# Optimization experiments

Hardware: AMD Instinct MI355X
Metric: run time of the kernel (lower is better)

Reference implementation:

```python
import jax, jax.numpy as jnp
import numpy as np

B, H, W, C = 4, 224, 224, 256
HEADS = 8
WIN = 7
N = WIN * WIN  # 49 tokens per window
MLP_HID = 4 * C
EPS = 1e-5


def _rel_index(w):
    coords = np.stack(np.meshgrid(np.arange(w), np.arange(w), indexing='ij'))  # (2,w,w)
    cf = coords.reshape(2, -1)                       # (2, w*w)
    rc = cf[:, :, None] - cf[:, None, :]             # (2, N, N)
    rc = rc.transpose(1, 2, 0).astype(np.int64)      # (N, N, 2)
    rc[:, :, 0] += w - 1
    rc[:, :, 1] += w - 1
    rc[:, :, 0] *= 2 * w - 1
    return jnp.asarray(rc.sum(-1), dtype=jnp.int32)  # (N, N)


def setup_inputs() -> dict:
    key = jax.random.key(0)
    ks = jax.random.split(key, 6)
    std = 0.02
    return {
        'x': jax.random.normal(ks[0], (B, H, W, C), dtype=jnp.float32),
        'norm1_g': jnp.ones((C,), jnp.float32),
        'norm1_b': jnp.zeros((C,), jnp.float32),
        'qkv_w': jax.random.normal(ks[1], (3 * C, C), jnp.float32) * std,
        'qkv_b': jnp.zeros((3 * C,), jnp.float32),
        'bias_table': jax.random.normal(ks[2], ((2 * WIN - 1) ** 2, HEADS), jnp.float32) * std,
        'proj_w': jax.random.normal(ks[3], (C, C), jnp.float32) * std,
        'proj_b': jnp.zeros((C,), jnp.float32),
        'norm2_g': jnp.ones((C,), jnp.float32),
        'norm2_b': jnp.zeros((C,), jnp.float32),
        'fc1_w': jax.random.normal(ks[4], (MLP_HID, C), jnp.float32) * std,
        'fc1_b': jnp.zeros((MLP_HID,), jnp.float32),
        'fc2_w': jax.random.normal(ks[5], (C, MLP_HID), jnp.float32) * std,
        'fc2_b': jnp.zeros((C,), jnp.float32),
        'rel_index': _rel_index(WIN),
    }


def _layernorm(x, g, b):
    mu = jnp.mean(x, axis=-1, keepdims=True)
    var = jnp.mean(jnp.square(x - mu), axis=-1, keepdims=True)
    return (x - mu) * jax.lax.rsqrt(var + EPS) * g + b


def reference(x, norm1_g, norm1_b, qkv_w, qkv_b, bias_table, proj_w, proj_b,
              norm2_g, norm2_b, fc1_w, fc1_b, fc2_w, fc2_b, rel_index):
    Bc, Hc, Wc, Cc = x.shape
    d = Cc // HEADS
    scale = d ** -0.5
    nh, nw = Hc // WIN, Wc // WIN

    shortcut = x
    h = _layernorm(x, norm1_g, norm1_b)

    # window_partition: (B,H,W,C) -> (B*nW, N, C)
    wins = h.reshape(Bc, nh, WIN, nw, WIN, Cc).transpose(0, 1, 3, 2, 4, 5)
    wins = wins.reshape(-1, N, Cc)

    # qkv projection and split into heads
    qkv = wins @ qkv_w.T + qkv_b                                  # (Bw, N, 3C)
    qkv = qkv.reshape(-1, N, 3, HEADS, d).transpose(2, 0, 3, 1, 4)  # (3, Bw, h, N, d)
    q, k, v = qkv[0], qkv[1], qkv[2]

    attn = jnp.einsum('bhnd,bhmd->bhnm', q, k) * scale            # (Bw, h, N, N)
    bias = bias_table[rel_index.reshape(-1)].reshape(N, N, HEADS).transpose(2, 0, 1)
    attn = jax.nn.softmax(attn + bias[None], axis=-1)

    o = jnp.einsum('bhnm,bhmd->bhnd', attn, v)                    # (Bw, h, N, d)
    o = o.transpose(0, 2, 1, 3).reshape(-1, N, Cc)
    o = o @ proj_w.T + proj_b

    # window_reverse: (B*nW, N, C) -> (B,H,W,C)
    o = o.reshape(Bc, nh, nw, WIN, WIN, Cc).transpose(0, 1, 3, 2, 4, 5)
    o = o.reshape(Bc, Hc, Wc, Cc)

    x = shortcut + o
    h2 = _layernorm(x, norm2_g, norm2_b)
    m = jax.nn.gelu(h2 @ fc1_w.T + fc1_b, approximate=False) @ fc2_w.T + fc2_b
    return x + m
```

## Files before the change

### kernel.cpp

```cpp
#include <hip/hip_runtime.h>

typedef unsigned short u16;
typedef __bf16 bf16x8 __attribute__((ext_vector_type(8)));
typedef float f32x4 __attribute__((ext_vector_type(4)));

#define TOKENS 200704
#define QK_ELEMS 51380224UL

__device__ __forceinline__ u16 f2b(float f) {
    __bf16 h = (__bf16)f;
    return __builtin_bit_cast(u16, h);
}

__device__ __forceinline__ int win2tok(int gm) {
    const int win = gm / 49, pos = gm - win * 49;
    const int b = win >> 10, wrem = win & 1023, wy = wrem >> 5, wx = wrem & 31;
    const int y = wy * 7 + pos / 7, x = wx * 7 + pos % 7;
    return b * 50176 + y * 224 + x;
}

#define GLDS(g, l) __builtin_amdgcn_global_load_lds( \
    (const __attribute__((address_space(1))) void*)(g), \
    (__attribute__((address_space(3))) void*)(l), 16, 0, 0)

#define MFMA __builtin_amdgcn_mfma_f32_16x16x32_bf16

template<int EPI, int WR, int WC>
__global__ __launch_bounds__(512, 4)
void gemm_t(const u16* __restrict__ A, const u16* __restrict__ W,
            const float* __restrict__ bias, int nt, int K, long moff,
            u16* __restrict__ outb, float* __restrict__ outf,
            const float* __restrict__ res,
            const float* __restrict__ g2, const float* __restrict__ b2,
            u16* __restrict__ h2o)
{
    constexpr int BM = WR * 64, BN = WC * 64;
    constexpr int ACH = BM / 16;
    constexpr int TCH = (BM + BN) / 16;
    __shared__ u16 As[3][BM * 32];
    __shared__ u16 Bs[3][BN * 32];
    __shared__ float red[EPI == 1 ? 2 * 128 * 4 : 1];

    const int tid  = threadIdx.x;
    const int wave = tid >> 6, lane = tid & 63;

    const int nwg = gridDim.x, bidO = blockIdx.x;
    const int qq = nwg >> 3, rr = nwg & 7;
    const int xcd = bidO & 7, idxx = bidO >> 3;
    const int bid = (xcd < rr) ? (xcd * (qq + 1) + idxx)
                               : (rr * (qq + 1) + (xcd - rr) * qq + idxx);

    const int bm = bid / nt, bn = bid % nt;
    const long m0 = (long)bm * BM;
    const int  n0 = bn * BN;
    const int wr = wave / WC, wc = wave % WC;
    const int lr = lane & 15, lg = lane >> 4;
    const int ccol_s = (((lane & 3) ^ ((lane >> 3) & 3)) * 8);
    const int swzr = (lg ^ ((lr >> 1) & 3)) * 8;

    f32x4 acc[4][4] = {};

    auto stage = [&](int buf, int k0) {
#pragma unroll
        for (int p = 0; p < TCH / 8; ++p) {
            const int q = p * 8 + wave;
            const int rq = (q < ACH) ? q : q - ACH;
            const int row = rq * 16 + (lane >> 2);
            if (q < ACH)
                GLDS(A + (m0 + row) * (long)K + k0 + ccol_s, &As[buf][rq * 512]);
            else
                GLDS(W + (long)(n0 + row) * K + k0 + ccol_s, &Bs[buf][rq * 512]);
        }
    };

    auto compute = [&](int buf) {
        bf16x8 af[4], bfr[4];
#pragma unroll
        for (int fm = 0; fm < 4; ++fm)
            af[fm] = *reinterpret_cast<const bf16x8*>(
                &As[buf][(wr * 64 + fm * 16 + lr) * 32 + swzr]);
#pragma unroll
        for (int fn = 0; fn < 4; ++fn)
            bfr[fn] = *reinterpret_cast<const bf16x8*>(
                &Bs[buf][(wc * 64 + fn * 16 + lr) * 32 + swzr]);
        __builtin_amdgcn_s_setprio(1);
#pragma unroll
        for (int fm = 0; fm < 4; ++fm)
#pragma unroll
            for (int fn = 0; fn < 4; ++fn)
                acc[fm][fn] = MFMA(af[fm], bfr[fn], acc[fm][fn], 0, 0, 0);
        __builtin_amdgcn_s_setprio(0);
    };

    const int nk = K >> 5;
    stage(0, 0);
    stage(1, 32);
    stage(2, 64);
    int k = 96;
    int buf = 0;
    for (int t = 0; t < nk; ++t) {
        if (t + 2 < nk)      asm volatile("s_waitcnt vmcnt(6)" ::: "memory");
        else if (t + 1 < nk) asm volatile("s_waitcnt vmcnt(3)" ::: "memory");
        else                 asm volatile("s_waitcnt vmcnt(0)" ::: "memory");
        __builtin_amdgcn_s_barrier();
        __builtin_amdgcn_sched_barrier(0);
        compute(buf);
        __builtin_amdgcn_s_barrier();
        __builtin_amdgcn_sched_barrier(0);
        if (t + 3 < nk) {
            stage(buf, k); k += 32;
            __builtin_amdgcn_sched_barrier(0);
        }
        buf = (buf == 2) ? 0 : buf + 1;
    }

    if constexpr (EPI == 0 || EPI == 2) {
        u16* st = &As[0][0];
        float bb4[4], sc4[4];
#pragma unroll
        for (int fn = 0; fn < 4; ++fn) {
            const int n = n0 + wc * 64 + fn * 16 + lr;
            bb4[fn] = bias[n];
            sc4[fn] = (EPI == 0 && (n >> 8) == 0) ? 0.17677669529663687f : 1.0f;
        }
        const size_t secbase = (EPI == 0)
            ? (size_t)(n0 >> 8) * QK_ELEMS + (size_t)(n0 & 255) : 0;
#pragma unroll
        for (int h = 0; h < 2; ++h) {
            if ((wr >> 1) == h) {
#pragma unroll
                for (int fm = 0; fm < 4; ++fm) {
#pragma unroll
                    for (int r = 0; r < 4; ++r) {
                        const int lrow = (wr & 1) * 64 + fm * 16 + lg * 4 + r;
                        const int swb = ((lrow >> 2) & 3) << 1;
#pragma unroll
                        for (int fn = 0; fn < 4; ++fn) {
                            const int col = wc * 64 + fn * 16 + lr;
                            const int cs = (col >> 3) ^ swb;
                            float v = acc[fm][fn][r] + bb4[fn];
                            u16 w;
                            if (EPI == 0) {
                                w = f2b(v * sc4[fn]);
                            } else {
                                const float s = v * (1.5957691216f + 0.07135481627f * v * v);
                                w = f2b(v * __builtin_amdgcn_rcpf(1.0f + __expf(-s)));
                            }
                            st[lrow * 128 + cs * 8 + (col & 7)] = w;
                        }
                    }
                }
            }
            asm volatile("s_waitcnt lgkmcnt(0)" ::: "memory");
            __builtin_amdgcn_s_barrier();
#pragma unroll
            for (int it = 0; it < 4; ++it) {
                const int u = it * 512 + tid;
                const int row = u >> 4, chunk = u & 15;
                const int cs = chunk ^ (((row >> 2) & 3) << 1);
                const bf16x8 val = *reinterpret_cast<const bf16x8*>(st + row * 128 + cs * 8);
                const long m = m0 + h * 128 + row;
                if (EPI == 0) {
                    *reinterpret_cast<bf16x8*>(outb + secbase + m * 256 + (chunk << 3)) = val;
                } else {
                    *reinterpret_cast<bf16x8*>(outb + m * 1024 + n0 + (chunk << 3)) = val;
                }
            }
            if (h == 0) {
                asm volatile("s_waitcnt lgkmcnt(0)" ::: "memory");
                __builtin_amdgcn_s_barrier();
            }
        }
    } else if constexpr (EPI == 1) {
        float g2c[4], b2c[4];
#pragma unroll
        for (int fn = 0; fn < 4; ++fn) {
            const int n = wc * 64 + fn * 16 + lr;
            g2c[fn] = g2[n]; b2c[fn] = b2[n];
        }
#pragma unroll
        for (int fm = 0; fm < 4; ++fm) {
#pragma unroll
            for (int r = 0; r < 4; ++r) {
                const long m = m0 + wr * 64 + fm * 16 + lg * 4 + r;
                const size_t trow = (size_t)win2tok((int)m) * 256;
                float s = 0.f, s2 = 0.f;
#pragma unroll
                for (int fn = 0; fn < 4; ++fn) {
                    const int n = wc * 64 + fn * 16 + lr;
                    const float x2 = acc[fm][fn][r] + bias[n] + res[trow + n];
                    acc[fm][fn][r] = x2;
                    outf[trow + n] = x2;
                    s += x2; s2 += x2 * x2;
                }
#pragma unroll
                for (int d = 1; d < 16; d <<= 1) { s += __shfl_xor(s, d); s2 += __shfl_xor(s2, d); }
                if (lr == 0) {
                    const int tok = wr * 64 + fm * 16 + lg * 4 + r;
                    red[(0 * 128 + tok) * 4 + wc] = s;
                    red[(1 * 128 + tok) * 4 + wc] = s2;
                }
            }
        }
        __syncthreads();
#pragma unroll
        for (int fm = 0; fm < 4; ++fm) {
#pragma unroll
            for (int r = 0; r < 4; ++r) {
                const int tok = wr * 64 + fm * 16 + lg * 4 + r;
                const float s = red[(0 * 128 + tok) * 4 + 0] + red[(0 * 128 + tok) * 4 + 1]
                              + red[(0 * 128 + tok) * 4 + 2] + red[(0 * 128 + tok) * 4 + 3];
                const float q = red[(1 * 128 + tok) * 4 + 0] + red[(1 * 128 + tok) * 4 + 1]
                              + red[(1 * 128 + tok) * 4 + 2] + red[(1 * 128 + tok) * 4 + 3];
                const float mu = s * 0.00390625f;
                const float rs = rsqrtf(q * 0.00390625f - mu * mu + 1e-5f);
                const long m = m0 + tok;
#pragma unroll
                for (int fn = 0; fn < 4; ++fn) {
                    const int n = wc * 64 + fn * 16 + lr;
                    h2o[m * 256 + n] = f2b((acc[fm][fn][r] - mu) * rs * g2c[fn] + b2c[fn]);
                }
            }
        }
    } else {
#pragma unroll
        for (int fm = 0; fm < 4; ++fm) {
#pragma unroll
            for (int r = 0; r < 4; ++r) {
                const long m = m0 + wr * 64 + fm * 16 + lg * 4 + r;
                const size_t trow = (size_t)win2tok((int)(m + moff)) * 256;
#pragma unroll
                for (int fn = 0; fn < 4; ++fn) {
                    const int n = n0 + wc * 64 + fn * 16 + lr;
                    outf[trow + n] += acc[fm][fn][r] + bias[n];
                }
            }
        }
    }
}

__global__ __launch_bounds__(256)
void layernorm_k(const float* __restrict__ in, const float* __restrict__ g,
                 const float* __restrict__ bb, u16* __restrict__ out)
{
    const int token = blockIdx.x * 4 + (threadIdx.x >> 6);
    const int lane = threadIdx.x & 63;
    const float4 v = *reinterpret_cast<const float4*>(in + (size_t)token * 256 + lane * 4);
    float s  = v.x + v.y + v.z + v.w;
    float s2 = v.x * v.x + v.y * v.y + v.z * v.z + v.w * v.w;
#pragma unroll
    for (int m = 1; m < 64; m <<= 1) { s += __shfl_xor(s, m); s2 += __shfl_xor(s2, m); }
    const float mu  = s * (1.0f / 256.0f);
    const float var = s2 * (1.0f / 256.0f) - mu * mu;
    const float rs  = rsqrtf(var + 1e-5f);
    const float4 gv = *reinterpret_cast<const float4*>(g + lane * 4);
    const float4 bv = *reinterpret_cast<const float4*>(bb + lane * 4);
    ushort4 o;
    o.x = f2b((v.x - mu) * rs * gv.x + bv.x);
    o.y = f2b((v.y - mu) * rs * gv.y + bv.y);
    o.z = f2b((v.z - mu) * rs * gv.z + bv.z);
    o.w = f2b((v.w - mu) * rs * gv.w + bv.w);
    const int b = token / 50176, rem = token % 50176;
    const int y = rem / 224, x = rem % 224;
    const int win = (b * 32 + y / 7) * 32 + x / 7;
    const int pos = (y % 7) * 7 + (x % 7);
    const size_t wrow = (size_t)win * 49 + pos;
    *reinterpret_cast<ushort4*>(out + wrow * 256 + lane * 4) = o;
}

__global__ __launch_bounds__(256)
void attn_win(const u16* __restrict__ qkv, const float* __restrict__ biasF,
              u16* __restrict__ outb)
{
    __shared__ u16 plds[4][64 * 72];
    __shared__ u16 vlds[4][2048];
    const int wave = threadIdx.x >> 6, lane = threadIdx.x & 63;
    const int pair = blockIdx.x * 4 + wave;
    const int head = pair & 7, win = pair >> 3;
    const int lr = lane & 15, lg = lane >> 4;

    const u16* Q  = qkv + (size_t)win * 12544 + head * 32;
    const u16* Kp = Q + QK_ELEMS;
    const u16* Vp = Q + 2 * QK_ELEMS;

    bf16x8 qf[4], kf[4];
#pragma unroll
    for (int f = 0; f < 4; ++f) {
        int n = f * 16 + lr; n = n > 48 ? 48 : n;
        qf[f] = *reinterpret_cast<const bf16x8*>(Q  + n * 256 + lg * 8);
        kf[f] = *reinterpret_cast<const bf16x8*>(Kp + n * 256 + lg * 8);
    }

    u16* vl = &vlds[wave][0];
    {
        const int posh = lane >> 1, dsub = (lane & 1) * 8;
#pragma unroll
        for (int db = 0; db < 2; ++db)
#pragma unroll
            for (int half = 0; half < 2; ++half) {
                int pos = half * 32 + posh; if (pos > 48) pos = 48;
                GLDS(Vp + pos * 256 + db * 16 + dsub, vl + db * 1024 + half * 512);
            }
    }

    f32x4 s[4][4] = {};
#pragma unroll
    for (int fm = 0; fm < 4; ++fm)
#pragma unroll
        for (int fn = 0; fn < 4; ++fn)
            s[fm][fn] = MFMA(qf[fm], kf[fn], s[fm][fn], 0, 0, 0);

    const float* bfh = biasF + head * 4096;
    u16* pl = &plds[wave][0];
#pragma unroll
    for (int fm = 0; fm < 4; ++fm) {
        f32x4 bb[4];
#pragma unroll
        for (int fn = 0; fn < 4; ++fn)
            bb[fn] = *reinterpret_cast<const f32x4*>(bfh + ((fm * 4 + fn) << 8) + (lane << 2));
#pragma unroll
        for (int r = 0; r < 4; ++r) {
            const int row = fm * 16 + lg * 4 + r;
            float v0 = s[fm][0][r] + bb[0][r];
            float v1 = s[fm][1][r] + bb[1][r];
            float v2 = s[fm][2][r] + bb[2][r];
            float v3 = s[fm][3][r] + bb[3][r];
            float mx = fmaxf(fmaxf(v0, v1), fmaxf(v2, v3));
#pragma unroll
            for (int d = 1; d < 16; d <<= 1) mx = fmaxf(mx, __shfl_xor(mx, d));
            const float p0 = __expf(v0 - mx), p1 = __expf(v1 - mx);
            const float p2 = __expf(v2 - mx), p3 = __expf(v3 - mx);
            float sum = p0 + p1 + p2 + p3;
#pragma unroll
            for (int d = 1; d < 16; d <<= 1) sum += __shfl_xor(sum, d);
            const float rinv = __builtin_amdgcn_rcpf(sum);
            pl[row * 72 +  0 + lr] = f2b(p0 * rinv);
            pl[row * 72 + 16 + lr] = f2b(p1 * rinv);
            pl[row * 72 + 32 + lr] = f2b(p2 * rinv);
            pl[row * 72 + 48 + lr] = f2b(p3 * rinv);
        }
    }

    asm volatile("s_waitcnt vmcnt(0)" ::: "memory");
    if (lane < 60) {
        const int db = lane / 30, ix = lane % 30;
        f32x4 z = {0.f, 0.f, 0.f, 0.f};
        *reinterpret_cast<f32x4*>(vl + db * 1024 + 784 + ix * 8) = z;
    }
    asm volatile("s_waitcnt lgkmcnt(0)" ::: "memory");
    __builtin_amdgcn_sched_barrier(0);

    const unsigned VB = (unsigned)(unsigned long)
        (__attribute__((address_space(3))) u16*)vl;
    unsigned long long trv[2][2][2];
#pragma unroll
    for (int kc = 0; kc < 2; ++kc)
#pragma unroll
        for (int f2 = 0; f2 < 2; ++f2) {
            const unsigned va = VB + f2 * 2048 + kc * 1024 + lg * 256 + lr * 2;
            asm volatile("ds_read_b64_tr_b16 %0, %1"
                         : "=v"(trv[kc][f2][0]) : "v"(va));
            asm volatile("ds_read_b64_tr_b16 %0, %1 offset:128"
                         : "=v"(trv[kc][f2][1]) : "v"(va));
        }
    asm volatile("s_waitcnt lgkmcnt(0)" ::: "memory");
    __builtin_amdgcn_sched_barrier(0);

    f32x4 o[4][2] = {};
#pragma unroll
    for (int kc = 0; kc < 2; ++kc) {
#pragma unroll
        for (int fm = 0; fm < 4; ++fm) {
            const bf16x8 pa = *reinterpret_cast<const bf16x8*>(
                pl + (fm * 16 + lr) * 72 + kc * 32 + lg * 8);
#pragma unroll
            for (int f2 = 0; f2 < 2; ++f2) {
                union { unsigned long long q[2]; bf16x8 v; } u;
                u.q[0] = trv[kc][f2][0]; u.q[1] = trv[kc][f2][1];
                o[fm][f2] = MFMA(pa, u.v, o[fm][f2], 0, 0, 0);
            }
        }
    }

    u16* ob = outb + (size_t)win * 12544 + head * 32;
#pragma unroll
    for (int fm = 0; fm < 4; ++fm) {
#pragma unroll
        for (int r = 0; r < 4; ++r) {
            const int tok = fm * 16 + lg * 4 + r;
            if (tok > 48) continue;
#pragma unroll
            for (int f2 = 0; f2 < 2; ++f2)
                ob[tok * 256 + f2 * 16 + lr] = f2b(o[fm][f2][r]);
        }
    }
}

__global__ __launch_bounds__(256)
void prep(const float* __restrict__ qw, const float* __restrict__ pw,
          const float* __restrict__ f1, const float* __restrict__ f2,
          u16* __restrict__ outw,
          const float* __restrict__ btab, const int* __restrict__ relidx,
          float* __restrict__ biasF)
{
    if (blockIdx.x < 3072) {
        const int t = blockIdx.x * 256 + threadIdx.x;
        float v;
        if (t < 196608) v = qw[t];
        else if (t < 262144) v = pw[t - 196608];
        else if (t < 524288) v = f1[t - 262144];
        else v = f2[t - 524288];
        outw[t] = f2b(v);
    } else {
        const int t = (blockIdx.x - 3072) * 256 + threadIdx.x;
        const int head = t >> 10, rem = t & 1023;
        const int fr = rem >> 6, lane = rem & 63;
        const int fm = fr >> 2, fn = fr & 3;
        const int lr = lane & 15, lg = lane >> 4;
        const int col = fn * 16 + lr;
        f32x4 o;
#pragma unroll
        for (int r = 0; r < 4; ++r) {
            int row = fm * 16 + lg * 4 + r; if (row > 48) row = 48;
            o[r] = (col > 48) ? -1e30f : btab[relidx[row * 49 + col] * 8 + head];
        }
        *reinterpret_cast<f32x4*>(biasF + t * 4) = o;
    }
}

extern "C" void kernel_launch(void* const* d_in, const int* in_sizes, int n_in,
                              void* d_out, int out_size, void* d_ws, size_t ws_size,
                              hipStream_t stream)
{
    const float* x      = (const float*)d_in[0];
    const float* n1g    = (const float*)d_in[1];
    const float* n1b    = (const float*)d_in[2];
    const float* qkv_w  = (const float*)d_in[3];
    const float* qkv_b  = (const float*)d_in[4];
    const float* btab   = (const float*)d_in[5];
    const float* proj_w = (const float*)d_in[6];
    const float* proj_b = (const float*)d_in[7];
    const float* n2g    = (const float*)d_in[8];
    const float* n2b    = (const float*)d_in[9];
    const float* fc1_w  = (const float*)d_in[10];
    const float* fc1_b  = (const float*)d_in[11];
    const float* fc2_w  = (const float*)d_in[12];
    const float* fc2_b  = (const float*)d_in[13];
    const int*   relidx = (const int*)d_in[14];
    float* out = (float*)d_out;

    char* ws = (char*)d_ws;
    u16*   wbf   = (u16*)ws;
    float* biasF = (float*)(ws + 1572864);
    u16*   hbuf  = (u16*)(ws + 1703936);
    u16*   rbuf  = (u16*)(ws + 1703936 + 102760448);
    const size_t r_avail = ws_size - (1703936 + 102760448);

    const u16* Wq  = wbf;
    const u16* Wp  = wbf + 196608;
    const u16* Wf1 = wbf + 262144;
    const u16* Wf2 = wbf + 524288;

    prep<<<3104, 256, 0, stream>>>(qkv_w, proj_w, fc1_w, fc2_w, wbf,
                                   btab, relidx, biasF);
    layernorm_k<<<50176, 256, 0, stream>>>(x, n1g, n1b, hbuf);

    gemm_t<0, 4, 2><<<784 * 6, 512, 0, stream>>>(hbuf, Wq, qkv_b, 6, 256, 0,
                                                 rbuf, nullptr, nullptr, nullptr, nullptr, nullptr);
    attn_win<<<8192, 256, 0, stream>>>(rbuf, biasF, hbuf);

    gemm_t<1, 2, 4><<<1568, 512, 0, stream>>>(hbuf, Wp, proj_b, 1, 256, 0,
                                              nullptr, out, x, n2g, n2b, hbuf);

    long rows_per = 50176;
    if ((long)(r_avail / 2048) < rows_per) rows_per = 25088;
    for (long r0 = 0; r0 < TOKENS; r0 += rows_per) {
        const long rows = (TOKENS - r0 < rows_per) ? (TOKENS - r0) : rows_per;
        gemm_t<2, 4, 2><<<(int)((rows / 256) * 8), 512, 0, stream>>>(
            hbuf + r0 * 256, Wf1, fc1_b, 8, 256, 0, rbuf, nullptr, nullptr, nullptr, nullptr, nullptr);
        gemm_t<3, 4, 2><<<(int)((rows / 256) * 2), 512, 0, stream>>>(
            rbuf, Wf2, fc2_b, 2, 1024, r0, nullptr, out, nullptr, nullptr, nullptr, nullptr);
    }
}
```

Baseline: 994.1 us.

## Add dedicated fc2 GEMM kernel with full-width N tiles and triple buffering

Replaces the generic gemm_t used for the fc2 projection with a specialised kernel in which each workgroup computes a 256x256 output tile covering the whole N dimension. The A activations are therefore read once rather than twice. K tiles are staged through a three-deep LDS ring, with global loads interleaved between MFMA groups and priority raised around the MFMAs. It also remaps blocks across XCDs. The larger accumulator tile raises register pressure and halves the grid size, which may reduce occupancy.

After: 1.022 ms. 2.8% more time.

```diff
diff --git a/kernel.cpp b/kernel.cpp
--- a/kernel.cpp
+++ b/kernel.cpp
@@ -222,18 +222,109 @@
                 }
             }
         }
-    } else {
-#pragma unroll
-        for (int fm = 0; fm < 4; ++fm) {
-#pragma unroll
-            for (int r = 0; r < 4; ++r) {
-                const long m = m0 + wr * 64 + fm * 16 + lg * 4 + r;
-                const size_t trow = (size_t)win2tok((int)(m + moff)) * 256;
-#pragma unroll
-                for (int fn = 0; fn < 4; ++fn) {
-                    const int n = n0 + wc * 64 + fn * 16 + lr;
-                    outf[trow + n] += acc[fm][fn][r] + bias[n];
-                }
+    }
+}
+
+__global__ __launch_bounds__(512, 2)
+void fc2k(const u16* __restrict__ A, const u16* __restrict__ W,
+          const float* __restrict__ bias, int K, long moff,
+          float* __restrict__ outf)
+{
+    __shared__ u16 As3[3][256 * 32];
+    __shared__ u16 Bs3[3][256 * 32];
+    const int tid  = threadIdx.x;
+    const int wave = tid >> 6, lane = tid & 63;
+
+    const int nwg = gridDim.x, bidO = blockIdx.x;
+    const int qq = nwg >> 3, rr = nwg & 7;
+    const int xcd = bidO & 7, idxx = bidO >> 3;
+    const int bid = (xcd < rr) ? (xcd * (qq + 1) + idxx)
+                               : (rr * (qq + 1) + (xcd - rr) * qq + idxx);
+
+    const long m0 = (long)bid * 256;
+    const int wr = wave >> 2, wc = wave & 3;
+    const int lr = lane & 15, lg = lane >> 4;
+    const int ccol_s = (((lane & 3) ^ ((lane >> 3) & 3)) * 8);
+    const int swzr = (lg ^ ((lr >> 1) & 3)) * 8;
+
+    f32x4 acc[8][4] = {};
+
+    auto stageA = [&](int buf, int k0, int half) {
+        const int c = half * 8 + wave;
+        const int row = c * 16 + (lane >> 2);
+        GLDS(A + (m0 + row) * (long)K + k0 + ccol_s, &As3[buf][c * 512]);
+    };
+    auto stageB = [&](int buf, int k0, int half) {
+        const int c = half * 8 + wave;
+        const int row = c * 16 + (lane >> 2);
+        GLDS(W + (long)row * K + k0 + ccol_s, &Bs3[buf][c * 512]);
+    };
+
+    const int nk = K >> 5;
+    stageA(0, 0, 0);  stageB(0, 0, 0);  stageA(0, 0, 1);  stageB(0, 0, 1);
+    stageA(1, 32, 0); stageB(1, 32, 0); stageA(1, 32, 1); stageB(1, 32, 1);
+    int buf = 0, k = 64;
+    for (int t = 0; t < nk; ++t) {
+        if (t + 1 < nk) asm volatile("s_waitcnt vmcnt(4)" ::: "memory");
+        else            asm volatile("s_waitcnt vmcnt(0)" ::: "memory");
+        __builtin_amdgcn_s_barrier();
+        __builtin_amdgcn_sched_barrier(0);
+
+        const int sb = (buf == 0) ? 2 : buf - 1;
+        const bool doStage = (t + 2 < nk);
+        bf16x8 bfr[4], afA[2], afB[2];
+#pragma unroll
+        for (int fn = 0; fn < 4; ++fn)
+            bfr[fn] = *reinterpret_cast<const bf16x8*>(
+                &Bs3[buf][(wc * 64 + fn * 16 + lr) * 32 + swzr]);
+#pragma unroll
+        for (int p = 0; p < 2; ++p)
+            afA[p] = *reinterpret_cast<const bf16x8*>(
+                &As3[buf][(wr * 128 + p * 16 + lr) * 32 + swzr]);
+#pragma unroll
+        for (int q = 0; q < 4; ++q) {
+            bf16x8 (&cur)[2] = (q & 1) ? afB : afA;
+            bf16x8 (&nxt)[2] = (q & 1) ? afA : afB;
+            if (q < 3) {
+#pragma unroll
+                for (int p = 0; p < 2; ++p)
+                    nxt[p] = *reinterpret_cast<const bf16x8*>(
+                        &As3[buf][(wr * 128 + ((q + 1) * 2 + p) * 16 + lr) * 32 + swzr]);
+            }
+            if (doStage) {
+                if (q == 0)      stageA(sb, k, 0);
+                else if (q == 1) stageB(sb, k, 0);
+                else if (q == 2) stageA(sb, k, 1);
+                else             stageB(sb, k, 1);
+            }
+            __builtin_amdgcn_s_setprio(1);
+#pragma unroll
+            for (int p = 0; p < 2; ++p)
+#pragma unroll
+                for (int fn = 0; fn < 4; ++fn)
+                    acc[q * 2 + p][fn] = MFMA(cur[p], bfr[fn], acc[q * 2 + p][fn], 0, 0, 0);
+            __builtin_amdgcn_s_setprio(0);
+        }
+        if (doStage) k += 32;
+        __builtin_amdgcn_s_barrier();
+        __builtin_amdgcn_sched_barrier(0);
+        buf = (buf == 2) ? 0 : buf + 1;
+    }
+
+    float bb4[4];
+#pragma unroll
+    for (int fn = 0; fn < 4; ++fn)
+        bb4[fn] = bias[wc * 64 + fn * 16 + lr];
+#pragma unroll
+    for (int fm = 0; fm < 8; ++fm) {
+#pragma unroll
+        for (int r = 0; r < 4; ++r) {
+            const long m = m0 + wr * 128 + fm * 16 + lg * 4 + r;
+            const size_t trow = (size_t)win2tok((int)(m + moff)) * 256;
+#pragma unroll
+            for (int fn = 0; fn < 4; ++fn) {
+                const int n = wc * 64 + fn * 16 + lr;
+                outf[trow + n] += acc[fm][fn][r] + bb4[fn];
             }
         }
     }
@@ -478,7 +569,7 @@
         const long rows = (TOKENS - r0 < rows_per) ? (TOKENS - r0) : rows_per;
         gemm_t<2, 4, 2><<<(int)((rows / 256) * 8), 512, 0, stream>>>(
             hbuf + r0 * 256, Wf1, fc1_b, 8, 256, 0, rbuf, nullptr, nullptr, nullptr, nullptr, nullptr);
-        gemm_t<3, 4, 2><<<(int)((rows / 256) * 2), 512, 0, stream>>>(
-            rbuf, Wf2, fc2_b, 2, 1024, r0, nullptr, out, nullptr, nullptr, nullptr, nullptr);
-    }
-}
+        fc2k<<<(int)(rows / 256), 512, 0, stream>>>(
+            rbuf, Wf2, fc2_b, 1024, r0, out);
+    }
+}
```
